# Optimization experiments

Measured on AMD Instinct MI355X. Metric: run time of the kernel, lower is better.

Reference implementation:

```python
import jax, jax.numpy as jnp
import numpy as np
from jax import lax

EPS = 1e-5
K = 13  # correlation window (pad 6 each side)

def _conv(x, w, b):
    # 3x3 conv, stride 1, padding 1, NCHW/OIHW
    y = lax.conv_general_dilated(x, w, (1, 1), ((1, 1), (1, 1)),
                                 dimension_numbers=('NCHW', 'OIHW', 'NCHW'))
    return y + b[None, :, None, None]

def _inorm(x):
    # InstanceNorm2d: per-sample per-channel, biased var, no affine
    m = jnp.mean(x, axis=(2, 3), keepdims=True)
    v = jnp.mean((x - m) ** 2, axis=(2, 3), keepdims=True)
    return (x - m) * lax.rsqrt(v + EPS)

def _block(x, wa, ba, wb, bb):
    x = jax.nn.relu(_conv(x, wa, ba))
    x = jax.nn.relu(_conv(x, wb, bb))
    return _inorm(x)

def _forward(color, corr, w1a, b1a, w1b, b1b, w2a, b2a, w2b, b2b,
             w3a, b3a, w3b, b3b, w4a, b4a, w4b, b4b, H, W):
    conv1 = _block(color[:, :, ::2, ::2], w1a, b1a, w1b, b1b)   # (B,64,2H,2W)
    conv2 = _block(conv1[:, :, ::2, ::2], w2a, b2a, w2b, b2b)   # (B,128,H,W)
    B, C = conv2.shape[0], conv2.shape[1]
    pad = jnp.pad(conv2, ((0, 0), (0, 0), (6, 6), (6, 6)), mode='edge')
    # 'pre' mode: content-adaptive 13x13 windowed weighted sum.
    # accumulating corr[:, t] * shifted-window of conv2_pad.
    def body(acc, t):
        i, j = t // K, t % K
        patch = lax.dynamic_slice(pad, (0, 0, i, j), (B, C, H, W))
        acc = acc + corr[:, t][:, None, :] * patch.reshape(B, C, H * W)
        return acc, None
    align, _ = lax.scan(body, jnp.zeros((B, C, H * W), conv2.dtype),
                        jnp.arange(K * K))
    align_1 = align.reshape(B, C, H, W)                          # (B,128,H,W)
    align_2 = _block(align_1[:, :, ::2, ::2], w3a, b3a, w3b, b3b)  # (B,256,H/2,W/2)
    align_3 = _block(align_2[:, :, ::2, ::2], w4a, b4a, w4b, b4b)  # (B,512,H/4,W/4)
    return (align_1, align_2, align_3)

def setup_inputs() -> dict:
    key = jax.random.key(0)
    ks = jax.random.split(key, 20)
    def w(k, shape):
        return jax.random.normal(k, shape, jnp.float32) * 0.05
    B, H, W = 4, 128, 128
    inp = {
        'color': jax.random.normal(ks[0], (B, 2, 4 * H, 4 * W), jnp.float32),
        'corr': jax.random.normal(ks[1], (B, K * K, H * W), jnp.float32) * 0.05,
        'w1a': w(ks[2], (64, 2, 3, 3)),    'b1a': jnp.zeros((64,), jnp.float32),
        'w1b': w(ks[3], (64, 64, 3, 3)),   'b1b': jnp.zeros((64,), jnp.float32),
        'w2a': w(ks[4], (128, 64, 3, 3)),  'b2a': jnp.zeros((128,), jnp.float32),
        'w2b': w(ks[5], (128, 128, 3, 3)), 'b2b': jnp.zeros((128,), jnp.float32),
        'w3a': w(ks[6], (256, 128, 3, 3)), 'b3a': jnp.zeros((256,), jnp.float32),
        'w3b': w(ks[7], (256, 256, 3, 3)), 'b3b': jnp.zeros((256,), jnp.float32),
        'w4a': w(ks[8], (512, 256, 3, 3)), 'b4a': jnp.zeros((512,), jnp.float32),
        'w4b': w(ks[9], (512, 512, 3, 3)), 'b4b': jnp.zeros((512,), jnp.float32),
        'H': H, 'W': W,
    }
    return inp

def reference(color, corr, w1a, b1a, w1b, b1b, w2a, b2a, w2b, b2b,
              w3a, b3a, w3b, b3b, w4a, b4a, w4b, b4b, H, W):
    return _forward(color, corr, w1a, b1a, w1b, b1b, w2a, b2a, w2b, b2b,
                    w3a, b3a, w3b, b3b, w4a, b4a, w4b, b4b, H, W)
```

## Files before the change

kernel.cpp:

```cpp
#include <hip/hip_runtime.h>
#include <hip/hip_bf16.h>

typedef __hip_bfloat16 bf16;
typedef __attribute__((ext_vector_type(8))) short short8;
typedef __attribute__((ext_vector_type(4))) float f32x4;

__device__ __forceinline__ float b2f(bf16 v) { return __bfloat162float(v); }
__device__ __forceinline__ bf16 f2b(float v) { return __float2bfloat16(v); }
__device__ __forceinline__ short fbits(float v) {
  bf16 h = f2b(v); return *reinterpret_cast<short*>(&h);
}
__device__ __forceinline__ float sb2f(short s) {
  return b2f(*reinterpret_cast<bf16*>(&s));
}
__device__ __forceinline__ int xcd_swz(int bid, int nwg) {
  int q = nwg >> 3, r = nwg & 7;
  int xcd = bid & 7, idx = bid >> 3;
  return (xcd < r ? xcd * (q + 1) : r * (q + 1) + (xcd - r) * q) + idx;
}

__global__ __launch_bounds__(256) void repack_k(
    const float* __restrict__ w, short* __restrict__ Wr, int Cin, int Cout)
{
  const int nkc = Cin >> 5, ncof = Cout >> 4;
  const size_t gid = (size_t)blockIdx.x * 256 + threadIdx.x;
  const int lane = gid & 63;
  size_t r = gid >> 6;
  const int tap = r % 9; r /= 9;
  const int kcc = r % nkc; r /= nkc;
  const int cof = r % ncof;
  const int hl = r / ncof;
  const int co = cof * 16 + (lane & 15);
  short8 v;
#pragma unroll
  for (int j = 0; j < 8; ++j) {
    int ci = kcc * 32 + ((lane >> 4) * 8 + j);
    float wv = w[((size_t)co * Cin + ci) * 9 + tap];
    bf16 hi = f2b(wv);
    v[j] = hl ? fbits(wv - b2f(hi)) : *reinterpret_cast<short*>(&hi);
  }
  *reinterpret_cast<short8*>(Wr + gid * 8) = v;
}

template<int R, int CX, int S>
__global__ __launch_bounds__(256) void conv_mfma_k(
    const bf16* __restrict__ src, bf16* __restrict__ dst,
    const short8* __restrict__ Wr, const float* __restrict__ bias,
    const float2* __restrict__ stats,
    int Win, int Hout, int Wout, int Cin, int Cout, int XT)
{
  constexpr int ROWS = R + 2;
  constexpr int COLS = CX + 2;
  constexpr int NGR = ROWS * 4 * COLS;
  __shared__ short8 a_s[NGR];

  const int b = blockIdx.z, cog = blockIdx.y;
  const int xt = blockIdx.x % XT, yt = blockIdx.x / XT;
  const int x0 = xt * CX, y0 = yt * R;
  const int tid = threadIdx.x, lane = tid & 63, wid = tid >> 6;
  const int wm = wid & 1, wn = wid >> 1;
  const int nkc = Cin >> 5;
  const int ncof = Cout >> 4;
  const int l15 = lane & 15, lg = lane >> 4;

  f32x4 acc[2][2] = {};

  int arow[2], acolb[2];
#pragma unroll
  for (int fm = 0; fm < 2; ++fm) {
    int p = wm * 32 + fm * 16 + l15;
    arow[fm] = p / CX;
    acolb[fm] = p % CX;
  }

  auto bload = [&](int hl, int fn, int kcc, int tap) -> short8 {
    int cof = cog * 4 + wn * 2 + fn;
    return Wr[((((size_t)hl * ncof + cof) * nkc + kcc) * 9 + tap) * 64 + lane];
  };
  auto gload = [&](int kcc, int idx) -> short8 {
    int g = idx & 3, cix = idx >> 2;
    int col = cix % COLS, row = cix / COLS;
    int sy = y0 + row - 1;
    int sx = x0 + col - 1;
    short8 v = {};
    if (sy >= 0 && sy < Hout && sx >= 0 && sx < Wout) {
      int ry = S ? 2 * sy : sy, rx = S ? 2 * sx : sx;
      v = *reinterpret_cast<const short8*>(
          reinterpret_cast<const short*>(src) +
          (((size_t)b * (S ? 2 * Hout : Hout) + ry) * Win + rx) * Cin +
          kcc * 32 + g * 8);
      if (stats) {
        const float2* st = stats + (size_t)b * Cin + kcc * 32 + g * 8;
#pragma unroll
        for (int j = 0; j < 8; ++j)
          v[j] = fbits((sb2f(v[j]) - st[j].x) * st[j].y);
      }
    }
    return v;
  };
  auto slot_of = [&](int idx) -> int {
    int g = idx & 3, cix = idx >> 2;
    int col = cix % COLS, row = cix / COLS;
    return (row * 4 + g) * COLS + col;
  };

  short8 bc00 = bload(0, 0, 0, 0), bc01 = bload(0, 1, 0, 0);
  short8 bc10 = bload(1, 0, 0, 0), bc11 = bload(1, 1, 0, 0);

  {
    short8 s0 = {}, s1 = {};
    if (tid < NGR) s0 = gload(0, tid);
    if (tid + 256 < NGR) s1 = gload(0, tid + 256);
    if (tid < NGR) a_s[slot_of(tid)] = s0;
    if (tid + 256 < NGR) a_s[slot_of(tid + 256)] = s1;
  }
  __syncthreads();

  for (int kc = 0; kc < nkc; ++kc) {
    short8 s0 = {}, s1 = {};
    const bool more = (kc + 1 < nkc);
    if (more) {
      if (tid < NGR) s0 = gload(kc + 1, tid);
      if (tid + 256 < NGR) s1 = gload(kc + 1, tid + 256);
    }

#pragma unroll
    for (int tap = 0; tap < 9; ++tap) {
      const int dy = tap / 3, dx = tap % 3;
      int nt = tap + 1, nk = kc;
      if (nt == 9) { nt = 0; nk = (kc + 1 < nkc) ? kc + 1 : 0; }
      short8 bn00 = bload(0, 0, nk, nt), bn01 = bload(0, 1, nk, nt);
      short8 bn10 = bload(1, 0, nk, nt), bn11 = bload(1, 1, nk, nt);
      short8 a0 = a_s[((arow[0] + dy) * 4 + lg) * COLS + acolb[0] + dx];
      short8 a1 = a_s[((arow[1] + dy) * 4 + lg) * COLS + acolb[1] + dx];
      acc[0][0] = __builtin_amdgcn_mfma_f32_16x16x32_bf16(a0, bc00, acc[0][0], 0, 0, 0);
      acc[0][0] = __builtin_amdgcn_mfma_f32_16x16x32_bf16(a0, bc10, acc[0][0], 0, 0, 0);
      acc[0][1] = __builtin_amdgcn_mfma_f32_16x16x32_bf16(a0, bc01, acc[0][1], 0, 0, 0);
      acc[0][1] = __builtin_amdgcn_mfma_f32_16x16x32_bf16(a0, bc11, acc[0][1], 0, 0, 0);
      acc[1][0] = __builtin_amdgcn_mfma_f32_16x16x32_bf16(a1, bc00, acc[1][0], 0, 0, 0);
      acc[1][0] = __builtin_amdgcn_mfma_f32_16x16x32_bf16(a1, bc10, acc[1][0], 0, 0, 0);
      acc[1][1] = __builtin_amdgcn_mfma_f32_16x16x32_bf16(a1, bc01, acc[1][1], 0, 0, 0);
      acc[1][1] = __builtin_amdgcn_mfma_f32_16x16x32_bf16(a1, bc11, acc[1][1], 0, 0, 0);
      bc00 = bn00; bc01 = bn01; bc10 = bn10; bc11 = bn11;
    }

    if (more) {
      __syncthreads();
      if (tid < NGR) a_s[slot_of(tid)] = s0;
      if (tid + 256 < NGR) a_s[slot_of(tid + 256)] = s1;
      __syncthreads();
    }
  }

#pragma unroll
  for (int fn = 0; fn < 2; ++fn) {
    int co = cog * 64 + wn * 32 + fn * 16 + l15;
    float bs = bias[co];
#pragma unroll
    for (int fm = 0; fm < 2; ++fm) {
#pragma unroll
      for (int j = 0; j < 4; ++j) {
        int p = wm * 32 + fm * 16 + lg * 4 + j;
        int r = p / CX, x = p % CX;
        float v = fmaxf(acc[fm][fn][j] + bs, 0.f);
        dst[((size_t)(b * Hout + y0 + r) * Wout + x0 + x) * Cout + co] = f2b(v);
      }
    }
  }
}

__global__ __launch_bounds__(256) void conv1a_k(
    const float* __restrict__ src, bf16* __restrict__ dst,
    const float* __restrict__ w, const float* __restrict__ bias)
{
  const int b = blockIdx.z, cog = blockIdx.y;
  const int ty0 = (blockIdx.x / 16) * 16, tx0 = (blockIdx.x % 16) * 16;
  const int tid = threadIdx.x, tx = tid & 15, ty = tid >> 4;

  __shared__ float in_s[2][18][18];
  __shared__ __align__(16) float w_s[2][3][3][16];

  for (int idx = tid; idx < 2 * 324; idx += 256) {
    int ci = idx / 324, r = idx - ci * 324;
    int iy = r / 18, ix = r - iy * 18;
    int gy = ty0 + iy - 1, gx = tx0 + ix - 1;
    float v = 0.f;
    if (gy >= 0 && gy < 256 && gx >= 0 && gx < 256)
      v = src[((size_t)(b * 2 + ci) * 512 + 2 * gy) * 512 + 2 * gx];
    in_s[ci][iy][ix] = v;
  }
  for (int idx = tid; idx < 2 * 144; idx += 256) {
    int co = idx & 15, r = idx >> 4;
    int ci = r / 9, k = r - ci * 9;
    w_s[ci][k / 3][k % 3][co] = w[(size_t)((cog * 16 + co) * 2 + ci) * 9 + k];
  }
  __syncthreads();

  float acc[16];
#pragma unroll
  for (int i = 0; i < 16; ++i) acc[i] = 0.f;
  for (int ci = 0; ci < 2; ++ci)
#pragma unroll
    for (int dy = 0; dy < 3; ++dy)
#pragma unroll
      for (int dx = 0; dx < 3; ++dx) {
        float v = in_s[ci][ty + dy][tx + dx];
        const float4* wv = (const float4*)(&w_s[ci][dy][dx][0]);
        float4 w0 = wv[0], w1 = wv[1], w2 = wv[2], w3 = wv[3];
        acc[0] = fmaf(v, w0.x, acc[0]);   acc[1] = fmaf(v, w0.y, acc[1]);
        acc[2] = fmaf(v, w0.z, acc[2]);   acc[3] = fmaf(v, w0.w, acc[3]);
        acc[4] = fmaf(v, w1.x, acc[4]);   acc[5] = fmaf(v, w1.y, acc[5]);
        acc[6] = fmaf(v, w1.z, acc[6]);   acc[7] = fmaf(v, w1.w, acc[7]);
        acc[8] = fmaf(v, w2.x, acc[8]);   acc[9] = fmaf(v, w2.y, acc[9]);
        acc[10] = fmaf(v, w2.z, acc[10]); acc[11] = fmaf(v, w2.w, acc[11]);
        acc[12] = fmaf(v, w3.x, acc[12]); acc[13] = fmaf(v, w3.y, acc[13]);
        acc[14] = fmaf(v, w3.z, acc[14]); acc[15] = fmaf(v, w3.w, acc[15]);
      }

  const int gy = ty0 + ty, gx = tx0 + tx;
  short8 s0, s1;
#pragma unroll
  for (int j = 0; j < 8; ++j) {
    s0[j] = fbits(fmaxf(acc[j] + bias[cog * 16 + j], 0.f));
    s1[j] = fbits(fmaxf(acc[8 + j] + bias[cog * 16 + 8 + j], 0.f));
  }
  short8* dp = reinterpret_cast<short8*>(
      reinterpret_cast<short*>(dst) + (((size_t)(b * 256 + gy) * 256 + gx) * 64 + cog * 16));
  dp[0] = s0; dp[1] = s1;
}

__global__ __launch_bounds__(256) void inorm_stats1_k(
    const bf16* __restrict__ x, float2* __restrict__ part,
    int HW, int C, int nb, int PC)
{
  const int b = blockIdx.y, pc = blockIdx.x;
  const int NC8 = C >> 3;
  const int pgc = 256 / NC8;
  const int c8 = (threadIdx.x % NC8) * 8;
  const int pg = threadIdx.x / NC8;
  const int chunk = HW / PC;
  const int p0 = pc * chunk;

  float s[8] = {}, ss[8] = {};
  for (int p = p0 + pg; p < p0 + chunk; p += pgc) {
    short8 v = *reinterpret_cast<const short8*>(
        reinterpret_cast<const short*>(x) + ((size_t)b * HW + p) * C + c8);
#pragma unroll
    for (int j = 0; j < 8; ++j) {
      float f = sb2f(v[j]);
      s[j] += f; ss[j] += f * f;
    }
  }
  __shared__ float sh[2][2048];
#pragma unroll
  for (int j = 0; j < 8; ++j) {
    sh[0][pg * C + c8 + j] = s[j];
    sh[1][pg * C + c8 + j] = ss[j];
  }
  __syncthreads();
  for (int c = threadIdx.x; c < C; c += 256) {
    float as = 0.f, aq = 0.f;
    for (int g = 0; g < pgc; ++g) { as += sh[0][g * C + c]; aq += sh[1][g * C + c]; }
    part[((size_t)pc * nb + b) * C + c] = make_float2(as, aq);
  }
}

__global__ __launch_bounds__(256) void inorm_stats2_k(
    const float2* __restrict__ part, float2* __restrict__ stats,
    int HW, int C, int PC, int nb)
{
  const int b = blockIdx.y, cg = blockIdx.x;
  const int c = threadIdx.x & 63, i = threadIdx.x >> 6;
  float s = 0.f, ss = 0.f;
  for (int pc = i; pc < PC; pc += 4) {
    float2 v = part[((size_t)pc * nb + b) * C + cg * 64 + c];
    s += v.x; ss += v.y;
  }
  __shared__ float sh[2][4][64];
  sh[0][i][c] = s; sh[1][i][c] = ss;
  __syncthreads();
  if (threadIdx.x < 64) {
    int cc = threadIdx.x;
    float s4 = sh[0][0][cc] + sh[0][1][cc] + sh[0][2][cc] + sh[0][3][cc];
    float q4 = sh[1][0][cc] + sh[1][1][cc] + sh[1][2][cc] + sh[1][3][cc];
    float m = s4 / (float)HW;
    float var = q4 / (float)HW - m * m;
    stats[(size_t)b * C + cg * 64 + cc] = make_float2(m, rsqrtf(var + 1e-5f));
  }
}

__global__ __launch_bounds__(256) void inorm_apply_k(
    const bf16* __restrict__ x, const float2* __restrict__ stats, int HW, int C,
    bf16* __restrict__ dnhwc, float* __restrict__ fnchw)
{
  const int b = blockIdx.z, cg = blockIdx.y;
  const int c = cg * 64 + (threadIdx.x & 63);
  const int p = blockIdx.x * 4 + (threadIdx.x >> 6);
  const float2 st = stats[(size_t)b * C + c];
  const size_t ia = ((size_t)b * HW + p) * C + c;
  const float v = (b2f(x[ia]) - st.x) * st.y;
  if (dnhwc) dnhwc[ia] = f2b(v);
  if (fnchw) fnchw[((size_t)(b * C + c)) * HW + p] = v;
}

__global__ __launch_bounds__(256) void inorm_apply_pad_k(
    const bf16* __restrict__ x, const float2* __restrict__ stats,
    bf16* __restrict__ pad)
{
  const int b = blockIdx.z, cg = blockIdx.y, yy = blockIdx.x;
  const int tid = threadIdx.x;
  __shared__ bf16 t_s[64][130];
  __shared__ float2 st_s[64];
  if (tid < 64) st_s[tid] = stats[(size_t)b * 128 + cg * 64 + tid];
  __syncthreads();

  const int c8 = (tid & 7) * 8, px0 = tid >> 3;
#pragma unroll
  for (int pass = 0; pass < 4; ++pass) {
    int px = pass * 32 + px0;
    short8 v = *reinterpret_cast<const short8*>(
        reinterpret_cast<const short*>(x) +
        ((size_t)(b * 16384 + yy * 128 + px) * 128 + cg * 64 + c8));
#pragma unroll
    for (int j = 0; j < 8; ++j) {
      float2 st = st_s[c8 + j];
      t_s[c8 + j][px] = f2b((sb2f(v[j]) - st.x) * st.y);
    }
  }
  __syncthreads();

  for (int idx = tid; idx < 64 * 18; idx += 256) {
    int c = idx / 18, g = idx - (idx / 18) * 18;
    short8 v;
#pragma unroll
    for (int j = 0; j < 8; ++j) {
      int xx = g * 8 + j - 6;
      xx = xx < 0 ? 0 : (xx > 127 ? 127 : xx);
      v[j] = *reinterpret_cast<short*>(&t_s[c][xx]);
    }
    *reinterpret_cast<short8*>(
        reinterpret_cast<short*>(pad) +
        ((size_t)(b * 128 + cg * 64 + c) * 128 + yy) * 144 + g * 8) = v;
  }
}

__global__ __launch_bounds__(256) void corr_mfma_k(
    const float* __restrict__ corr, const bf16* __restrict__ pad,
    float* __restrict__ outc, bf16* __restrict__ outn, int b0)
{
  __shared__ __align__(16) char smem[26 * 64 * 16];
  short8* a_lds = reinterpret_cast<short8*>(smem);
  float* out_s = reinterpret_cast<float*>(smem);

  const int b = b0 + blockIdx.z;
  const int wg = xcd_swz(blockIdx.x, gridDim.x);
  const int y = wg >> 3, xt = wg & 7;
  const int x0 = xt * 16;
  const int tid = threadIdx.x, lane = tid & 63, wid = tid >> 6;
  const int l15 = lane & 15, lg = lane >> 4;

  for (int idx = tid; idx < 26 * 64; idx += 256) {
    short8 z = {};
    a_lds[idx] = z;
  }
  __syncthreads();

  unsigned short* ah = reinterpret_cast<unsigned short*>(a_lds);
  for (int idx = tid; idx < 169 * 16; idx += 256) {
    int t = idx >> 4, m = idx & 15;
    int dy = t / 13, dx = t - dy * 13;
    float f = corr[((size_t)b * 169 + t) * 16384 + y * 128 + x0 + m];
    bf16 hi = f2b(f);
    unsigned short hb = *reinterpret_cast<unsigned short*>(&hi);
    unsigned short lb = (unsigned short)fbits(f - b2f(hi));
    int k = m + dx;
    int ent = dy * 64 + (k >> 3) * 16 + m;
    ah[ent * 8 + (k & 7)] = hb;
    ah[(13 * 64 + ent) * 8 + (k & 7)] = lb;
  }
  __syncthreads();

  const int cg0 = wid * 2;
  f32x4 acc0 = {}, acc1 = {};
  const short* pb = reinterpret_cast<const short*>(pad);

  for (int dy = 0; dy < 13; ++dy) {
    int rowc = y + dy - 6; rowc = rowc < 0 ? 0 : (rowc > 127 ? 127 : rowc);
    short8 bhi = a_lds[dy * 64 + lane];
    short8 blo = a_lds[(13 + dy) * 64 + lane];
    size_t base0 = ((size_t)(b * 128 + cg0 * 16 + l15) * 128 + rowc) * 144
                   + x0 + lg * 8;
    short8 a0 = *reinterpret_cast<const short8*>(pb + base0);
    short8 a1 = *reinterpret_cast<const short8*>(pb + base0 + (size_t)16 * 128 * 144);
    acc0 = __builtin_amdgcn_mfma_f32_16x16x32_bf16(a0, bhi, acc0, 0, 0, 0);
    acc1 = __builtin_amdgcn_mfma_f32_16x16x32_bf16(a1, bhi, acc1, 0, 0, 0);
    acc0 = __builtin_amdgcn_mfma_f32_16x16x32_bf16(a0, blo, acc0, 0, 0, 0);
    acc1 = __builtin_amdgcn_mfma_f32_16x16x32_bf16(a1, blo, acc1, 0, 0, 0);
  }
  __syncthreads();

#pragma unroll
  for (int cgi = 0; cgi < 2; ++cgi) {
    f32x4 a = cgi ? acc1 : acc0;
    float* dst4 = out_s + l15 * 132 + (cg0 + cgi) * 16 + lg * 4;
    *reinterpret_cast<f32x4*>(dst4) = a;
  }
  __syncthreads();

  {
    int px_ = tid >> 4, c8 = (tid & 15) * 8;
    const float* row = out_s + px_ * 132 + c8;
    short8 v;
#pragma unroll
    for (int j = 0; j < 8; ++j) v[j] = fbits(row[j]);
    *reinterpret_cast<short8*>(
        reinterpret_cast<short*>(outn) +
        ((size_t)(b * 16384 + y * 128 + x0 + px_)) * 128 + c8) = v;
  }
  {
    int ch = tid >> 1, pg = tid & 1;
    float v0[4], v1[4];
#pragma unroll
    for (int i = 0; i < 4; ++i) v0[i] = out_s[(pg * 8 + i) * 132 + ch];
#pragma unroll
    for (int i = 0; i < 4; ++i) v1[i] = out_s[(pg * 8 + 4 + i) * 132 + ch];
    float* dst = outc + ((size_t)(b * 128 + ch)) * 16384 + y * 128 + x0 + pg * 8;
    *reinterpret_cast<float4*>(dst) = make_float4(v0[0], v0[1], v0[2], v0[3]);
    *reinterpret_cast<float4*>(dst + 4) = make_float4(v1[0], v1[1], v1[2], v1[3]);
  }
}

extern "C" void kernel_launch(void* const* d_in, const int* in_sizes, int n_in,
                              void* d_out, int out_size, void* d_ws, size_t ws_size,
                              hipStream_t stream) {
  const float* color = (const float*)d_in[0];
  const float* corr  = (const float*)d_in[1];
  const float* w1a = (const float*)d_in[2];  const float* b1a = (const float*)d_in[3];
  const float* w1b = (const float*)d_in[4];  const float* b1b = (const float*)d_in[5];
  const float* w2a = (const float*)d_in[6];  const float* b2a = (const float*)d_in[7];
  const float* w2b = (const float*)d_in[8];  const float* b2b = (const float*)d_in[9];
  const float* w3a = (const float*)d_in[10]; const float* b3a = (const float*)d_in[11];
  const float* w3b = (const float*)d_in[12]; const float* b3b = (const float*)d_in[13];
  const float* w4a = (const float*)d_in[14]; const float* b4a = (const float*)d_in[15];
  const float* w4b = (const float*)d_in[16]; const float* b4b = (const float*)d_in[17];

  float* out = (float*)d_out;
  char* ws = (char*)d_ws;
  const size_t MB = 1048576;
  float2* stats = (float2*)ws;
  float2* part  = (float2*)(ws + (64 << 10));
  short*  WrS   = (short*)(ws + (256 << 10));
  const short8* Wr = (const short8*)WrS;
  bf16* P0 = (bf16*)(ws + 10 * MB);
  bf16* P1 = (bf16*)(ws + 27 * MB);
  bf16* P2 = (bf16*)(ws + 44 * MB);
  bf16* X1 = P0;
  bf16* X2 = (bf16*)d_out;
  const float2* nost = (const float2*)nullptr;

  conv1a_k<<<dim3(256, 4, 4), 256, 0, stream>>>(color, X1, w1a, b1a);
  repack_k<<<36, 256, 0, stream>>>(w1b, WrS, 64, 64);
  conv_mfma_k<4, 16, 0><<<dim3(64 * 16, 1, 4), 256, 0, stream>>>(
      X1, X2, Wr, b1b, nost, 256, 256, 256, 64, 64, 16);
  inorm_stats1_k<<<dim3(64, 4), 256, 0, stream>>>(X2, part, 65536, 64, 4, 64);
  inorm_stats2_k<<<dim3(1, 4), 256, 0, stream>>>(part, stats, 65536, 64, 64, 4);

  repack_k<<<72, 256, 0, stream>>>(w2a, WrS, 64, 128);
  conv_mfma_k<4, 16, 1><<<dim3(32 * 8, 2, 4), 256, 0, stream>>>(
      X2, P0, Wr, b2a, stats, 256, 128, 128, 64, 128, 8);
  repack_k<<<144, 256, 0, stream>>>(w2b, WrS, 128, 128);
  conv_mfma_k<4, 16, 0><<<dim3(32 * 8, 2, 4), 256, 0, stream>>>(
      P0, P1, Wr, b2b, nost, 128, 128, 128, 128, 128, 8);
  inorm_stats1_k<<<dim3(64, 4), 256, 0, stream>>>(P1, part, 16384, 128, 4, 64);
  inorm_stats2_k<<<dim3(2, 4), 256, 0, stream>>>(part, stats, 16384, 128, 64, 4);
  inorm_apply_pad_k<<<dim3(128, 2, 4), 256, 0, stream>>>(P1, stats, P2);

  corr_mfma_k<<<dim3(128 * 8, 1, 2), 256, 0, stream>>>(corr, P2, out, P0, 0);
  corr_mfma_k<<<dim3(128 * 8, 1, 2), 256, 0, stream>>>(corr, P2, out, P0, 2);

  repack_k<<<288, 256, 0, stream>>>(w3a, WrS, 128, 256);
  conv_mfma_k<4, 16, 1><<<dim3(16 * 4, 4, 4), 256, 0, stream>>>(
      P0, P1, Wr, b3a, nost, 128, 64, 64, 128, 256, 4);
  repack_k<<<576, 256, 0, stream>>>(w3b, WrS, 256, 256);
  conv_mfma_k<4, 16, 0><<<dim3(16 * 4, 4, 4), 256, 0, stream>>>(
      P1, P2, Wr, b3b, nost, 64, 64, 64, 256, 256, 4);
  inorm_stats1_k<<<dim3(32, 4), 256, 0, stream>>>(P2, part, 4096, 256, 4, 32);
  inorm_stats2_k<<<dim3(4, 4), 256, 0, stream>>>(part, stats, 4096, 256, 32, 4);
  inorm_apply_k<<<dim3(1024, 4, 4), 256, 0, stream>>>(
      P2, stats, 4096, 256, (bf16*)nullptr, out + 8388608);

  repack_k<<<1152, 256, 0, stream>>>(w4a, WrS, 256, 512);
  conv_mfma_k<4, 16, 1><<<dim3(8 * 2, 8, 4), 256, 0, stream>>>(
      P2, P1, Wr, b4a, stats, 64, 32, 32, 256, 512, 2);
  repack_k<<<2304, 256, 0, stream>>>(w4b, WrS, 512, 512);
  conv_mfma_k<4, 16, 0><<<dim3(8 * 2, 8, 4), 256, 0, stream>>>(
      P1, P2, Wr, b4b, nost, 32, 32, 32, 512, 512, 2);
  inorm_stats1_k<<<dim3(32, 4), 256, 0, stream>>>(P2, part, 1024, 512, 4, 32);
  inorm_stats2_k<<<dim3(8, 4), 256, 0, stream>>>(part, stats, 1024, 512, 32, 4);
  inorm_apply_k<<<dim3(256, 8, 4), 256, 0, stream>>>(
      P2, stats, 1024, 512, (bf16*)nullptr, out + 12582912);
}
```

Measured before the change: 498.1 us.

## Enlarge conv spatial tiles to raise weight reuse, drop register prefetch of activations

Generalizes the MFMA conv kernel so each wave covers FM 16-pixel fragments rather than a fixed two, and launches with 16-row (or 8-row) tiles instead of 4-row tiles. Each weight fragment loaded from global memory is therefore reused across more output pixels, and the halo overhead per tile shrinks. The activation staging loop is simplified to a synchronous load-to-LDS per channel chunk, which removes the previous register-level prefetch overlap. Grids become much smaller, so occupancy and load balance on the deeper layers may suffer, and the larger accumulator arrays raise register pressure.

```diff
diff --git a/kernel.cpp b/kernel.cpp
--- a/kernel.cpp
+++ b/kernel.cpp
@@ -52,6 +52,7 @@
   constexpr int ROWS = R + 2;
   constexpr int COLS = CX + 2;
   constexpr int NGR = ROWS * 4 * COLS;
+  constexpr int FM = (R * CX) / 32;
   __shared__ short8 a_s[NGR];
 
   const int b = blockIdx.z, cog = blockIdx.y;
@@ -63,12 +64,12 @@
   const int ncof = Cout >> 4;
   const int l15 = lane & 15, lg = lane >> 4;
 
-  f32x4 acc[2][2] = {};
-
-  int arow[2], acolb[2];
-#pragma unroll
-  for (int fm = 0; fm < 2; ++fm) {
-    int p = wm * 32 + fm * 16 + l15;
+  f32x4 acc[FM][2] = {};
+
+  int arow[FM], acolb[FM];
+#pragma unroll
+  for (int fm = 0; fm < FM; ++fm) {
+    int p = wm * (R * CX / 2) + fm * 16 + l15;
     arow[fm] = p / CX;
     acolb[fm] = p % CX;
   }
@@ -77,78 +78,53 @@
     int cof = cog * 4 + wn * 2 + fn;
     return Wr[((((size_t)hl * ncof + cof) * nkc + kcc) * 9 + tap) * 64 + lane];
   };
-  auto gload = [&](int kcc, int idx) -> short8 {
-    int g = idx & 3, cix = idx >> 2;
-    int col = cix % COLS, row = cix / COLS;
-    int sy = y0 + row - 1;
-    int sx = x0 + col - 1;
-    short8 v = {};
-    if (sy >= 0 && sy < Hout && sx >= 0 && sx < Wout) {
-      int ry = S ? 2 * sy : sy, rx = S ? 2 * sx : sx;
-      v = *reinterpret_cast<const short8*>(
-          reinterpret_cast<const short*>(src) +
-          (((size_t)b * (S ? 2 * Hout : Hout) + ry) * Win + rx) * Cin +
-          kcc * 32 + g * 8);
-      if (stats) {
-        const float2* st = stats + (size_t)b * Cin + kcc * 32 + g * 8;
-#pragma unroll
-        for (int j = 0; j < 8; ++j)
-          v[j] = fbits((sb2f(v[j]) - st[j].x) * st[j].y);
+
+  short8 bc[2][2], bn_[2][2];
+  bc[0][0] = bload(0, 0, 0, 0); bc[0][1] = bload(0, 1, 0, 0);
+  bc[1][0] = bload(1, 0, 0, 0); bc[1][1] = bload(1, 1, 0, 0);
+
+  for (int kc = 0; kc < nkc; ++kc) {
+    __syncthreads();
+    for (int idx = tid; idx < NGR; idx += 256) {
+      int g = idx & 3, cix = idx >> 2;
+      int col = cix % COLS, row = cix / COLS;
+      int sy = y0 + row - 1;
+      int sx = x0 + col - 1;
+      short8 v = {};
+      if (sy >= 0 && sy < Hout && sx >= 0 && sx < Wout) {
+        int ry = S ? 2 * sy : sy, rx = S ? 2 * sx : sx;
+        v = *reinterpret_cast<const short8*>(
+            reinterpret_cast<const short*>(src) +
+            (((size_t)b * (S ? 2 * Hout : Hout) + ry) * Win + rx) * Cin +
+            kc * 32 + g * 8);
+        if (stats) {
+          const float2* st = stats + (size_t)b * Cin + kc * 32 + g * 8;
+#pragma unroll
+          for (int j = 0; j < 8; ++j)
+            v[j] = fbits((sb2f(v[j]) - st[j].x) * st[j].y);
+        }
       }
-    }
-    return v;
-  };
-  auto slot_of = [&](int idx) -> int {
-    int g = idx & 3, cix = idx >> 2;
-    int col = cix % COLS, row = cix / COLS;
-    return (row * 4 + g) * COLS + col;
-  };
-
-  short8 bc00 = bload(0, 0, 0, 0), bc01 = bload(0, 1, 0, 0);
-  short8 bc10 = bload(1, 0, 0, 0), bc11 = bload(1, 1, 0, 0);
-
-  {
-    short8 s0 = {}, s1 = {};
-    if (tid < NGR) s0 = gload(0, tid);
-    if (tid + 256 < NGR) s1 = gload(0, tid + 256);
-    if (tid < NGR) a_s[slot_of(tid)] = s0;
-    if (tid + 256 < NGR) a_s[slot_of(tid + 256)] = s1;
-  }
-  __syncthreads();
-
-  for (int kc = 0; kc < nkc; ++kc) {
-    short8 s0 = {}, s1 = {};
-    const bool more = (kc + 1 < nkc);
-    if (more) {
-      if (tid < NGR) s0 = gload(kc + 1, tid);
-      if (tid + 256 < NGR) s1 = gload(kc + 1, tid + 256);
-    }
+      a_s[(row * 4 + g) * COLS + col] = v;
+    }
+    __syncthreads();
 
 #pragma unroll
     for (int tap = 0; tap < 9; ++tap) {
       const int dy = tap / 3, dx = tap % 3;
       int nt = tap + 1, nk = kc;
       if (nt == 9) { nt = 0; nk = (kc + 1 < nkc) ? kc + 1 : 0; }
-      short8 bn00 = bload(0, 0, nk, nt), bn01 = bload(0, 1, nk, nt);
-      short8 bn10 = bload(1, 0, nk, nt), bn11 = bload(1, 1, nk, nt);
-      short8 a0 = a_s[((arow[0] + dy) * 4 + lg) * COLS + acolb[0] + dx];
-      short8 a1 = a_s[((arow[1] + dy) * 4 + lg) * COLS + acolb[1] + dx];
-      acc[0][0] = __builtin_amdgcn_mfma_f32_16x16x32_bf16(a0, bc00, acc[0][0], 0, 0, 0);
-      acc[0][0] = __builtin_amdgcn_mfma_f32_16x16x32_bf16(a0, bc10, acc[0][0], 0, 0, 0);
-      acc[0][1] = __builtin_amdgcn_mfma_f32_16x16x32_bf16(a0, bc01, acc[0][1], 0, 0, 0);
-      acc[0][1] = __builtin_amdgcn_mfma_f32_16x16x32_bf16(a0, bc11, acc[0][1], 0, 0, 0);
-      acc[1][0] = __builtin_amdgcn_mfma_f32_16x16x32_bf16(a1, bc00, acc[1][0], 0, 0, 0);
-      acc[1][0] = __builtin_amdgcn_mfma_f32_16x16x32_bf16(a1, bc10, acc[1][0], 0, 0, 0);
-      acc[1][1] = __builtin_amdgcn_mfma_f32_16x16x32_bf16(a1, bc01, acc[1][1], 0, 0, 0);
-      acc[1][1] = __builtin_amdgcn_mfma_f32_16x16x32_bf16(a1, bc11, acc[1][1], 0, 0, 0);
-      bc00 = bn00; bc01 = bn01; bc10 = bn10; bc11 = bn11;
-    }
-
-    if (more) {
-      __syncthreads();
-      if (tid < NGR) a_s[slot_of(tid)] = s0;
-      if (tid + 256 < NGR) a_s[slot_of(tid + 256)] = s1;
-      __syncthreads();
+      bn_[0][0] = bload(0, 0, nk, nt); bn_[0][1] = bload(0, 1, nk, nt);
+      bn_[1][0] = bload(1, 0, nk, nt); bn_[1][1] = bload(1, 1, nk, nt);
+#pragma unroll
+      for (int fm = 0; fm < FM; ++fm) {
+        short8 a = a_s[((arow[fm] + dy) * 4 + lg) * COLS + acolb[fm] + dx];
+        acc[fm][0] = __builtin_amdgcn_mfma_f32_16x16x32_bf16(a, bc[0][0], acc[fm][0], 0, 0, 0);
+        acc[fm][0] = __builtin_amdgcn_mfma_f32_16x16x32_bf16(a, bc[1][0], acc[fm][0], 0, 0, 0);
+        acc[fm][1] = __builtin_amdgcn_mfma_f32_16x16x32_bf16(a, bc[0][1], acc[fm][1], 0, 0, 0);
+        acc[fm][1] = __builtin_amdgcn_mfma_f32_16x16x32_bf16(a, bc[1][1], acc[fm][1], 0, 0, 0);
+      }
+      bc[0][0] = bn_[0][0]; bc[0][1] = bn_[0][1];
+      bc[1][0] = bn_[1][0]; bc[1][1] = bn_[1][1];
     }
   }
 
@@ -157,10 +133,10 @@
     int co = cog * 64 + wn * 32 + fn * 16 + l15;
     float bs = bias[co];
 #pragma unroll
-    for (int fm = 0; fm < 2; ++fm) {
+    for (int fm = 0; fm < FM; ++fm) {
 #pragma unroll
       for (int j = 0; j < 4; ++j) {
-        int p = wm * 32 + fm * 16 + lg * 4 + j;
+        int p = wm * (R * CX / 2) + fm * 16 + lg * 4 + j;
         int r = p / CX, x = p % CX;
         float v = fmaxf(acc[fm][fn][j] + bs, 0.f);
         dst[((size_t)(b * Hout + y0 + r) * Wout + x0 + x) * Cout + co] = f2b(v);
@@ -460,16 +436,16 @@
 
   conv1a_k<<<dim3(256, 4, 4), 256, 0, stream>>>(color, X1, w1a, b1a);
   repack_k<<<36, 256, 0, stream>>>(w1b, WrS, 64, 64);
-  conv_mfma_k<4, 16, 0><<<dim3(64 * 16, 1, 4), 256, 0, stream>>>(
+  conv_mfma_k<16, 16, 0><<<dim3(256, 1, 4), 256, 0, stream>>>(
       X1, X2, Wr, b1b, nost, 256, 256, 256, 64, 64, 16);
   inorm_stats1_k<<<dim3(64, 4), 256, 0, stream>>>(X2, part, 65536, 64, 4, 64);
   inorm_stats2_k<<<dim3(1, 4), 256, 0, stream>>>(part, stats, 65536, 64, 64, 4);
 
   repack_k<<<72, 256, 0, stream>>>(w2a, WrS, 64, 128);
-  conv_mfma_k<4, 16, 1><<<dim3(32 * 8, 2, 4), 256, 0, stream>>>(
+  conv_mfma_k<16, 16, 1><<<dim3(64, 2, 4), 256, 0, stream>>>(
       X2, P0, Wr, b2a, stats, 256, 128, 128, 64, 128, 8);
   repack_k<<<144, 256, 0, stream>>>(w2b, WrS, 128, 128);
-  conv_mfma_k<4, 16, 0><<<dim3(32 * 8, 2, 4), 256, 0, stream>>>(
+  conv_mfma_k<16, 16, 0><<<dim3(64, 2, 4), 256, 0, stream>>>(
       P0, P1, Wr, b2b, nost, 128, 128, 128, 128, 128, 8);
   inorm_stats1_k<<<dim3(64, 4), 256, 0, stream>>>(P1, part, 16384, 128, 4, 64);
   inorm_stats2_k<<<dim3(2, 4), 256, 0, stream>>>(part, stats, 16384, 128, 64, 4);
@@ -479,10 +455,10 @@
   corr_mfma_k<<<dim3(128 * 8, 1, 2), 256, 0, stream>>>(corr, P2, out, P0, 2);
 
   repack_k<<<288, 256, 0, stream>>>(w3a, WrS, 128, 256);
-  conv_mfma_k<4, 16, 1><<<dim3(16 * 4, 4, 4), 256, 0, stream>>>(
+  conv_mfma_k<16, 16, 1><<<dim3(16, 4, 4), 256, 0, stream>>>(
       P0, P1, Wr, b3a, nost, 128, 64, 64, 128, 256, 4);
   repack_k<<<576, 256, 0, stream>>>(w3b, WrS, 256, 256);
-  conv_mfma_k<4, 16, 0><<<dim3(16 * 4, 4, 4), 256, 0, stream>>>(
+  conv_mfma_k<16, 16, 0><<<dim3(16, 4, 4), 256, 0, stream>>>(
       P1, P2, Wr, b3b, nost, 64, 64, 64, 256, 256, 4);
   inorm_stats1_k<<<dim3(32, 4), 256, 0, stream>>>(P2, part, 4096, 256, 4, 32);
   inorm_stats2_k<<<dim3(4, 4), 256, 0, stream>>>(part, stats, 4096, 256, 32, 4);
@@ -490,10 +466,10 @@
       P2, stats, 4096, 256, (bf16*)nullptr, out + 8388608);
 
   repack_k<<<1152, 256, 0, stream>>>(w4a, WrS, 256, 512);
-  conv_mfma_k<4, 16, 1><<<dim3(8 * 2, 8, 4), 256, 0, stream>>>(
+  conv_mfma_k<8, 16, 1><<<dim3(8, 8, 4), 256, 0, stream>>>(
       P2, P1, Wr, b4a, stats, 64, 32, 32, 256, 512, 2);
   repack_k<<<2304, 256, 0, stream>>>(w4b, WrS, 512, 512);
-  conv_mfma_k<4, 16, 0><<<dim3(8 * 2, 8, 4), 256, 0, stream>>>(
+  conv_mfma_k<8, 16, 0><<<dim3(8, 8, 4), 256, 0, stream>>>(
       P1, P2, Wr, b4b, nost, 32, 32, 32, 512, 512, 2);
   inorm_stats1_k<<<dim3(32, 4), 256, 0, stream>>>(P2, part, 1024, 512, 4, 32);
   inorm_stats2_k<<<dim3(8, 4), 256, 0, stream>>>(part, stats, 1024, 512, 32, 4);
```

New measurement: 496.5 us. About the same (-0.3%).
